# Performance work log

Measured on AMD Instinct MI355X. Metric: run time of the kernel, lower is better.

Reference implementation:

```python
import jax, jax.numpy as jnp
import numpy as np

N, E, G = 50000, 800000, 128
F_IN, F0, D, NL, DN = 128, 256, 256, 4, 512


def setup_inputs() -> dict:
    key = jax.random.key(0)
    ks = iter(jax.random.split(key, 40))

    def U(shape, fan_in):
        s = 1.0 / np.sqrt(fan_in)
        return jax.random.uniform(next(ks), shape, minval=-s, maxval=s, dtype=jnp.float32)

    x = jax.random.normal(next(ks), (N, F_IN), dtype=jnp.float32)
    edge_index = jax.random.randint(next(ks), (2, E), 0, N)
    batch_index = jnp.sort(jax.random.randint(next(ks), (N,), 0, G))
    return dict(
        x=x, edge_index=edge_index, batch_index=batch_index,
        fl_W=U((F_IN, F0), F_IN), fl_b=U((F0,), F_IN),
        conv1_W=U((F0, D), F0), conv1_b=U((D,), F0),
        tr1_W=U((D, D), D), tr1_b=U((D,), D),
        bn1_g=jnp.ones((D,), jnp.float32), bn1_b=jnp.zeros((D,), jnp.float32),
        convs_W=U((NL, D, D), D), convs_b=U((NL, D), D),
        trs_W=U((NL, D, D), D), trs_b=U((NL, D), D),
        bns_g=jnp.ones((NL, D), jnp.float32), bns_b=jnp.zeros((NL, D), jnp.float32),
        l1_W=U((2 * D, DN), 2 * D), l1_b=U((DN,), 2 * D),
        l2_W=U((DN, DN // 2), DN), l2_b=U((DN // 2,), DN),
        l3_W=U((DN // 2, 10), DN // 2), l3_b=U((10,), DN // 2),
    )


def reference(x, edge_index, batch_index, fl_W, fl_b, conv1_W, conv1_b,
              tr1_W, tr1_b, bn1_g, bn1_b, convs_W, convs_b, trs_W, trs_b,
              bns_g, bns_b, l1_W, l1_b, l2_W, l2_b, l3_W, l3_b):
    n = x.shape[0]
    loops = jnp.arange(n, dtype=edge_index.dtype)
    src = jnp.concatenate([edge_index[0], loops])  # [E+N] GCN self-loops
    dst = jnp.concatenate([edge_index[1], loops])
    deg = jax.ops.segment_sum(jnp.ones_like(dst, dtype=x.dtype), dst, num_segments=n)
    dis = jax.lax.rsqrt(deg)  # deg >= 1 due to self-loops
    norm = dis[src] * dis[dst]  # [E+N] symmetric normalization

    def gcn(h, W, b):
        m = h @ W
        return jax.ops.segment_sum(norm[:, None] * m[src], dst, num_segments=n) + b

    def bn(h, g, bb):
        mu = h.mean(axis=0)
        var = jnp.mean((h - mu) ** 2, axis=0)  # biased var, torch BN train math
        return g * (h - mu) * jax.lax.rsqrt(var + 1e-5) + bb

    h = x @ fl_W + fl_b
    h = jax.nn.relu(gcn(h, conv1_W, conv1_b))
    h = bn(h, bn1_g, bn1_b)
    h = jax.nn.relu(h @ tr1_W + tr1_b)  # dropout off (eval)
    for i in range(convs_W.shape[0]):
        h = jax.nn.relu(gcn(h, convs_W[i], convs_b[i]))
        h = bn(h, bns_g[i], bns_b[i])
        h = jax.nn.relu(h @ trs_W[i] + trs_b[i])

    sums = jax.ops.segment_sum(h, batch_index, num_segments=G)
    cnt = jax.ops.segment_sum(jnp.ones((n,), h.dtype), batch_index, num_segments=G)
    pooled = sums / jnp.maximum(cnt, 1.0)[:, None]  # global_mean_pool
    z = jnp.concatenate([pooled, pooled], axis=1)
    z = jax.nn.relu(z @ l1_W + l1_b)
    z = jax.nn.relu(z @ l2_W + l2_b)
    return z @ l3_W + l3_b
```

## Files before the change

kernel.cpp:

```cpp
#include <hip/hip_runtime.h>

#define DD 256

typedef unsigned short u16;
typedef unsigned int u32;
using bf16x8 = __attribute__((ext_vector_type(8))) short;
using f16x8  = __attribute__((ext_vector_type(8))) _Float16;
using f32x4  = __attribute__((ext_vector_type(4))) float;

#define GLB_PTR(p) ((const __attribute__((address_space(1))) u32*)(p))
#define LDS_PTR(p) ((__attribute__((address_space(3))) u32*)(p))


__device__ __forceinline__ u32 f2bfx2(float v) {
  u32 b = __float_as_uint(v);
  u32 hi = (b + 0x7fffu + ((b >> 16) & 1u)) >> 16;
  float hf = __uint_as_float(hi << 16);
  float lof = v - hf;
  u32 b2 = __float_as_uint(lof);
  u32 lo = (b2 + 0x7fffu + ((b2 >> 16) & 1u)) >> 16;
  return hi | (lo << 16);
}

__device__ __forceinline__ u16 f2h(float f) {
  _Float16 h = (_Float16)f;
  return __builtin_bit_cast(unsigned short, h);
}
__device__ __forceinline__ float h2f(u16 x) {
  return (float)__builtin_bit_cast(_Float16, x);
}

__device__ __forceinline__ bf16x8 as_bf16x8(uint4 u) {
  union { uint4 u; bf16x8 v; } c;
  c.u = u;
  return c.v;
}
__device__ __forceinline__ f16x8 as_f16x8(uint4 u) {
  union { uint4 u; f16x8 v; } c;
  c.u = u;
  return c.v;
}

__device__ __forceinline__ void unpack8(uint4 a, uint4 b, bf16x8& hi, bf16x8& lo) {
  union { u32 w[4]; bf16x8 v; } H, L;
  H.w[0] = __builtin_amdgcn_perm(a.y, a.x, 0x05040100u);
  L.w[0] = __builtin_amdgcn_perm(a.y, a.x, 0x07060302u);
  H.w[1] = __builtin_amdgcn_perm(a.w, a.z, 0x05040100u);
  L.w[1] = __builtin_amdgcn_perm(a.w, a.z, 0x07060302u);
  H.w[2] = __builtin_amdgcn_perm(b.y, b.x, 0x05040100u);
  L.w[2] = __builtin_amdgcn_perm(b.y, b.x, 0x07060302u);
  H.w[3] = __builtin_amdgcn_perm(b.w, b.z, 0x05040100u);
  L.w[3] = __builtin_amdgcn_perm(b.w, b.z, 0x07060302u);
  hi = H.v;
  lo = L.v;
}

__device__ __forceinline__ int packoff(int col, int k) {
  int w = col >> 6, r = (col >> 4) & 3, c16 = col & 15;
  int kc = k >> 5, q = (k >> 3) & 3, j = k & 7;
  return ((kc * 4 + w) * 4 + r) * 512 + (q * 16 + c16) * 8 + j;
}


__global__ void zero_i32_kernel(int* p, int n) {
  int i = blockIdx.x * 256 + threadIdx.x;
  if (i < n) p[i] = 0;
}

__global__ void zero_f32_kernel(float* p, int n) {
  int i = blockIdx.x * 256 + threadIdx.x;
  if (i < n) p[i] = 0.f;
}

__global__ void count_kernel(const int* __restrict__ dst, int* __restrict__ cnt, int e) {
  int i = blockIdx.x * 256 + threadIdx.x;
  if (i < e) atomicAdd(&cnt[dst[i]], 1);
}

__global__ void scan_block_kernel(const int* __restrict__ cnt, int* __restrict__ out,
                                  int* __restrict__ bsum, int n) {
  __shared__ int sh[256];
  int tid = threadIdx.x;
  int base = blockIdx.x * 1024 + tid * 4;
  int v0 = (base + 0 < n) ? cnt[base + 0] : 0;
  int v1 = (base + 1 < n) ? cnt[base + 1] : 0;
  int v2 = (base + 2 < n) ? cnt[base + 2] : 0;
  int v3 = (base + 3 < n) ? cnt[base + 3] : 0;
  int s = v0 + v1 + v2 + v3;
  sh[tid] = s;
  __syncthreads();
  for (int d = 1; d < 256; d <<= 1) {
    int t = (tid >= d) ? sh[tid - d] : 0;
    __syncthreads();
    sh[tid] += t;
    __syncthreads();
  }
  int excl = sh[tid] - s;
  if (base + 0 < n) out[base + 0] = excl;
  excl += v0;
  if (base + 1 < n) out[base + 1] = excl;
  excl += v1;
  if (base + 2 < n) out[base + 2] = excl;
  excl += v2;
  if (base + 3 < n) out[base + 3] = excl;
  if (tid == 255) bsum[blockIdx.x] = sh[255];
}

__global__ void scan_partials_kernel(int* bsum, int nb) {
  if (threadIdx.x == 0 && blockIdx.x == 0) {
    int acc = 0;
    for (int i = 0; i < nb; ++i) { int t = bsum[i]; bsum[i] = acc; acc += t; }
  }
}

__global__ void finalize_kernel(int* __restrict__ off, const int* __restrict__ bsum,
                                int* __restrict__ cursor, const int* __restrict__ cnt,
                                float* __restrict__ dis, int n, int e) {
  int i = blockIdx.x * 256 + threadIdx.x;
  if (i < n) {
    int o = off[i] + bsum[i >> 10];
    off[i] = o;
    cursor[i] = o;
    dis[i] = rsqrtf((float)(cnt[i] + 1));
  }
  if (i == 0 && blockIdx.x == 0) off[n] = e;
}

__global__ void fill_kernel(const int* __restrict__ src, const int* __restrict__ dst,
                            int* __restrict__ cursor, const float* __restrict__ dis,
                            int2* __restrict__ csrE, int e) {
  int i = blockIdx.x * 256 + threadIdx.x;
  if (i < e) {
    int s = src[i];
    int d = dst[i];
    int p = atomicAdd(&cursor[d], 1);
    float w = dis[s] * dis[d];
    csrE[p] = make_int2(s, __float_as_int(w));
  }
}


__global__ void xsplit_kernel(const float* __restrict__ x, u32* __restrict__ xq, int n) {
  int i = blockIdx.x * 256 + threadIdx.x;
  if (i < n) xq[i] = f2bfx2(x[i]);
}


__global__ void wsplit_all_kernel(const float* __restrict__ fl_W, const float* __restrict__ conv1_W,
                                  const float* __restrict__ convs_W, u16* __restrict__ flHi,
                                  u16* __restrict__ flLo, u16* __restrict__ cvF) {
  int j = blockIdx.x;
  int m = blockIdx.y;
  int k = threadIdx.x;
  if (m == 0) {
    if (k < 128) {
      u32 p = f2bfx2(fl_W[(size_t)k * 256 + j]);
      int off = packoff(j, k);
      flHi[off] = (u16)(p & 0xffffu);
      flLo[off] = (u16)(p >> 16);
    }
  } else {
    int c = m - 1;
    const float* W = (c == 0) ? conv1_W : convs_W + (size_t)(c - 1) * 65536;
    cvF[(size_t)c * 65536 + packoff(j, k)] = f2h(W[(size_t)k * 256 + j]);
  }
}

__global__ void wsplit_fold_kernel(const float* __restrict__ W, const float* __restrict__ scale,
                                   const float* __restrict__ shift, const float* __restrict__ bt,
                                   u16* __restrict__ trF, float* __restrict__ bias_out) {
  __shared__ float red[256];
  int j = blockIdx.x;
  int k = threadIdx.x;
  float w = W[(size_t)k * 256 + j];
  trF[packoff(j, k)] = f2h(w * scale[k]);
  red[k] = shift[k] * w;
  __syncthreads();
  for (int d = 128; d > 0; d >>= 1) {
    if (k < d) red[k] += red[k + d];
    __syncthreads();
  }
  if (k == 0) bias_out[j] = bt[j] + red[0];
}


__device__ __forceinline__ f16x8 afrag16(const u32* As, int R, int q) {
  int off = (q * 4) ^ (((R >> 1) & 3) << 2);
  return as_f16x8(*(const uint4*)(As + R * 16 + off));
}

__device__ __forceinline__ void afrag32(const u32* Asbase, int R, int q, bf16x8& ah, bf16x8& al) {
  int s = (R & 7) << 4;
  const u32* row = Asbase + R * 32;
  uint4 a0 = *(const uint4*)(row + ((((q * 32)) ^ s) >> 2));
  uint4 a1 = *(const uint4*)(row + ((((q * 32) + 16) ^ s) >> 2));
  unpack8(a0, a1, ah, al);
}

__global__ __launch_bounds__(256) void fused_fl_kernel(
    const u32* __restrict__ Aq, const u16* __restrict__ W1h, const u16* __restrict__ W1l,
    const float* __restrict__ bias1, const u16* __restrict__ W2f, u16* __restrict__ C,
    int nrows) {
  constexpr int NK1 = 4;
  __shared__ __align__(16) u32 As[2][2048];
  __shared__ __align__(16) u16 T[64 * 256];
  const int tid = threadIdx.x;
  const int lane = tid & 63;
  const int wave = tid >> 6;
  const int row0 = blockIdx.x * 64;
  const int q = lane >> 4;
  const int r16 = lane & 15;

  int sRowG[2], sOff[2];
#pragma unroll
  for (int c = 0; c < 2; ++c) {
    int row_l = c * 32 + wave * 8 + (lane >> 3);
    int grow = row0 + row_l;
    if (grow > nrows - 1) grow = nrows - 1;
    sRowG[c] = grow;
    sOff[c] = ((lane & 7) * 4) ^ ((row_l & 7) << 2);
  }

  int bBase[4];
#pragma unroll
  for (int r = 0; r < 4; ++r) bBase[r] = (wave * 4 + r) * 512 + lane * 8;

  f32x4 acc[4][4];
#pragma unroll
  for (int i = 0; i < 4; ++i)
#pragma unroll
    for (int r = 0; r < 4; ++r) acc[i][r] = (f32x4){0.f, 0.f, 0.f, 0.f};

  auto stage = [&](int buf, int kc32) {
#pragma unroll
    for (int c = 0; c < 2; ++c) {
      const u32* gsrc = Aq + (size_t)sRowG[c] * 128 + kc32 * 32 + sOff[c];
      u32* ldst = &As[buf][c * 1024 + wave * 256];
      __builtin_amdgcn_global_load_lds(GLB_PTR(gsrc), LDS_PTR(ldst), 16, 0, 0);
    }
  };

  stage(0, 0);
  __syncthreads();
  int buf = 0;
#pragma unroll
  for (int kc = 0; kc < NK1; ++kc) {
    if (kc + 1 < NK1) stage(buf ^ 1, kc + 1);
    uint4 BH[4], BL[4];
#pragma unroll
    for (int r = 0; r < 4; ++r) {
      BH[r] = *(const uint4*)(W1h + bBase[r] + kc * 8192);
      BL[r] = *(const uint4*)(W1l + bBase[r] + kc * 8192);
    }
    bf16x8 ah[4], al[4];
#pragma unroll
    for (int i = 0; i < 4; ++i) afrag32(As[buf], i * 16 + r16, q, ah[i], al[i]);
#pragma unroll
    for (int r = 0; r < 4; ++r) {
      bf16x8 bh = as_bf16x8(BH[r]);
      bf16x8 bl = as_bf16x8(BL[r]);
#pragma unroll
      for (int i = 0; i < 4; ++i) {
        acc[i][r] = __builtin_amdgcn_mfma_f32_16x16x32_bf16(ah[i], bh, acc[i][r], 0, 0, 0);
        acc[i][r] = __builtin_amdgcn_mfma_f32_16x16x32_bf16(al[i], bh, acc[i][r], 0, 0, 0);
        acc[i][r] = __builtin_amdgcn_mfma_f32_16x16x32_bf16(ah[i], bl, acc[i][r], 0, 0, 0);
      }
    }
    __syncthreads();
    buf ^= 1;
  }

#pragma unroll
  for (int r = 0; r < 4; ++r) {
    int col = wave * 64 + r * 16 + r16;
    float bv = bias1[col];
#pragma unroll
    for (int i = 0; i < 4; ++i) {
#pragma unroll
      for (int g = 0; g < 4; ++g) {
        int row = i * 16 + q * 4 + g;
        float v = acc[i][r][g] + bv;
        *(u16*)((char*)T + row * 512 + ((col * 2) ^ ((row & 7) << 4))) = f2h(v);
      }
    }
  }

#pragma unroll
  for (int i = 0; i < 4; ++i)
#pragma unroll
    for (int r = 0; r < 4; ++r) acc[i][r] = (f32x4){0.f, 0.f, 0.f, 0.f};
  __syncthreads();

#pragma unroll
  for (int kc = 0; kc < 8; ++kc) {
    uint4 BF[4];
#pragma unroll
    for (int r = 0; r < 4; ++r) BF[r] = *(const uint4*)(W2f + bBase[r] + kc * 8192);
    f16x8 af[4];
#pragma unroll
    for (int i = 0; i < 4; ++i) {
      int row = i * 16 + r16;
      int base = kc * 64 + q * 16;
      af[i] = as_f16x8(*(const uint4*)((char*)T + row * 512 + (base ^ ((row & 7) << 4))));
    }
#pragma unroll
    for (int r = 0; r < 4; ++r) {
      f16x8 bf = as_f16x8(BF[r]);
#pragma unroll
      for (int i = 0; i < 4; ++i)
        acc[i][r] = __builtin_amdgcn_mfma_f32_16x16x32_f16(af[i], bf, acc[i][r], 0, 0, 0);
    }
  }

#pragma unroll
  for (int r = 0; r < 4; ++r) {
    int col = wave * 64 + r * 16 + r16;
#pragma unroll
    for (int i = 0; i < 4; ++i) {
#pragma unroll
      for (int g = 0; g < 4; ++g) {
        int row = row0 + i * 16 + q * 4 + g;
        if (row < nrows) C[(size_t)row * 256 + col] = f2h(acc[i][r][g]);
      }
    }
  }
}

__global__ __launch_bounds__(256) void fused_h_kernel(
    const u16* __restrict__ Ah, const u16* __restrict__ W1f, const float* __restrict__ bias1,
    const u16* __restrict__ W2f, u16* __restrict__ C, int nrows) {
  __shared__ __align__(16) u32 As[2][1024];
  __shared__ __align__(16) u16 T[64 * 256];
  const int tid = threadIdx.x;
  const int lane = tid & 63;
  const int wave = tid >> 6;
  const int row0 = blockIdx.x * 64;
  const int q = lane >> 4;
  const int r16 = lane & 15;

  int row_l = tid >> 2;
  int grow = row0 + row_l;
  if (grow > nrows - 1) grow = nrows - 1;
  const int sK = (((tid & 3) * 8)) ^ (((row_l >> 1) & 3) << 3);

  int bBase[4];
#pragma unroll
  for (int r = 0; r < 4; ++r) bBase[r] = (wave * 4 + r) * 512 + lane * 8;

  f32x4 acc[4][4];
#pragma unroll
  for (int i = 0; i < 4; ++i)
#pragma unroll
    for (int r = 0; r < 4; ++r) acc[i][r] = (f32x4){0.f, 0.f, 0.f, 0.f};

  auto stage = [&](int buf, int kc32) {
    const u16* gsrc = Ah + (size_t)grow * 256 + kc32 * 32 + sK;
    u32* ldst = &As[buf][wave * 256];
    __builtin_amdgcn_global_load_lds(GLB_PTR(gsrc), LDS_PTR(ldst), 16, 0, 0);
  };

  stage(0, 0);
  __syncthreads();
  int buf = 0;
#pragma unroll
  for (int kc = 0; kc < 8; ++kc) {
    if (kc + 1 < 8) stage(buf ^ 1, kc + 1);
    uint4 BF[4];
#pragma unroll
    for (int r = 0; r < 4; ++r) BF[r] = *(const uint4*)(W1f + bBase[r] + kc * 8192);
    f16x8 af[4];
#pragma unroll
    for (int i = 0; i < 4; ++i) af[i] = afrag16(As[buf], i * 16 + r16, q);
#pragma unroll
    for (int r = 0; r < 4; ++r) {
      f16x8 bf = as_f16x8(BF[r]);
#pragma unroll
      for (int i = 0; i < 4; ++i)
        acc[i][r] = __builtin_amdgcn_mfma_f32_16x16x32_f16(af[i], bf, acc[i][r], 0, 0, 0);
    }
    __syncthreads();
    buf ^= 1;
  }

#pragma unroll
  for (int r = 0; r < 4; ++r) {
    int col = wave * 64 + r * 16 + r16;
    float bv = bias1[col];
#pragma unroll
    for (int i = 0; i < 4; ++i) {
#pragma unroll
      for (int g = 0; g < 4; ++g) {
        int row = i * 16 + q * 4 + g;
        float v = fmaxf(acc[i][r][g] + bv, 0.f);
        *(u16*)((char*)T + row * 512 + ((col * 2) ^ ((row & 7) << 4))) = f2h(v);
      }
    }
  }

#pragma unroll
  for (int i = 0; i < 4; ++i)
#pragma unroll
    for (int r = 0; r < 4; ++r) acc[i][r] = (f32x4){0.f, 0.f, 0.f, 0.f};
  __syncthreads();

#pragma unroll
  for (int kc = 0; kc < 8; ++kc) {
    uint4 BF[4];
#pragma unroll
    for (int r = 0; r < 4; ++r) BF[r] = *(const uint4*)(W2f + bBase[r] + kc * 8192);
    f16x8 af[4];
#pragma unroll
    for (int i = 0; i < 4; ++i) {
      int row = i * 16 + r16;
      int base = kc * 64 + q * 16;
      af[i] = as_f16x8(*(const uint4*)((char*)T + row * 512 + (base ^ ((row & 7) << 4))));
    }
#pragma unroll
    for (int r = 0; r < 4; ++r) {
      f16x8 bf = as_f16x8(BF[r]);
#pragma unroll
      for (int i = 0; i < 4; ++i)
        acc[i][r] = __builtin_amdgcn_mfma_f32_16x16x32_f16(af[i], bf, acc[i][r], 0, 0, 0);
    }
  }

#pragma unroll
  for (int r = 0; r < 4; ++r) {
    int col = wave * 64 + r * 16 + r16;
#pragma unroll
    for (int i = 0; i < 4; ++i) {
#pragma unroll
      for (int g = 0; g < 4; ++g) {
        int row = row0 + i * 16 + q * 4 + g;
        if (row < nrows) C[(size_t)row * 256 + col] = f2h(acc[i][r][g]);
      }
    }
  }
}

__global__ __launch_bounds__(256) void gemm_h_kernel(
    const u16* __restrict__ Ah, const u16* __restrict__ W1f, const float* __restrict__ bias,
    u16* __restrict__ C, int nrows) {
  __shared__ __align__(16) u32 As[2][1024];
  const int tid = threadIdx.x;
  const int lane = tid & 63;
  const int wave = tid >> 6;
  const int row0 = blockIdx.x * 64;
  const int q = lane >> 4;
  const int r16 = lane & 15;

  int row_l = tid >> 2;
  int grow = row0 + row_l;
  if (grow > nrows - 1) grow = nrows - 1;
  const int sK = (((tid & 3) * 8)) ^ (((row_l >> 1) & 3) << 3);

  int bBase[4];
#pragma unroll
  for (int r = 0; r < 4; ++r) bBase[r] = (wave * 4 + r) * 512 + lane * 8;

  f32x4 acc[4][4];
#pragma unroll
  for (int i = 0; i < 4; ++i)
#pragma unroll
    for (int r = 0; r < 4; ++r) acc[i][r] = (f32x4){0.f, 0.f, 0.f, 0.f};

  auto stage = [&](int buf, int kc32) {
    const u16* gsrc = Ah + (size_t)grow * 256 + kc32 * 32 + sK;
    u32* ldst = &As[buf][wave * 256];
    __builtin_amdgcn_global_load_lds(GLB_PTR(gsrc), LDS_PTR(ldst), 16, 0, 0);
  };

  stage(0, 0);
  __syncthreads();
  int buf = 0;
#pragma unroll
  for (int kc = 0; kc < 8; ++kc) {
    if (kc + 1 < 8) stage(buf ^ 1, kc + 1);
    uint4 BF[4];
#pragma unroll
    for (int r = 0; r < 4; ++r) BF[r] = *(const uint4*)(W1f + bBase[r] + kc * 8192);
    f16x8 af[4];
#pragma unroll
    for (int i = 0; i < 4; ++i) af[i] = afrag16(As[buf], i * 16 + r16, q);
#pragma unroll
    for (int r = 0; r < 4; ++r) {
      f16x8 bf = as_f16x8(BF[r]);
#pragma unroll
      for (int i = 0; i < 4; ++i)
        acc[i][r] = __builtin_amdgcn_mfma_f32_16x16x32_f16(af[i], bf, acc[i][r], 0, 0, 0);
    }
    __syncthreads();
    buf ^= 1;
  }

#pragma unroll
  for (int r = 0; r < 4; ++r) {
    int col = wave * 64 + r * 16 + r16;
    float bv = bias[col];
#pragma unroll
    for (int i = 0; i < 4; ++i) {
#pragma unroll
      for (int g = 0; g < 4; ++g) {
        int row = row0 + i * 16 + q * 4 + g;
        if (row < nrows) C[(size_t)row * 256 + col] = f2h(fmaxf(acc[i][r][g] + bv, 0.f));
      }
    }
  }
}


__global__ __launch_bounds__(256) void gather_kernel(
    const u16* __restrict__ m, const int* __restrict__ off,
    const int2* __restrict__ csrE, const float* __restrict__ dis,
    const float* __restrict__ bias, u16* __restrict__ out,
    float* __restrict__ shard, int n) {
  __shared__ float2 red[4][256];
  int wv = threadIdx.x >> 6;
  int lane = threadIdx.x & 63;
  int node = blockIdx.x * 4 + wv;
  float ax = 0.f, ay = 0.f, az = 0.f, aw = 0.f;
  if (node < n) {
    float di = dis[node];
    uint2 v = *(const uint2*)(m + (size_t)node * DD + lane * 4);
    float w = di * di;
    ax = w * h2f((u16)(v.x & 0xffff)); ay = w * h2f((u16)(v.x >> 16));
    az = w * h2f((u16)(v.y & 0xffff)); aw = w * h2f((u16)(v.y >> 16));
    int e0 = off[node], e1 = off[node + 1];
    int e = e0;
    for (; e + 3 < e1; e += 4) {
      int2 p0 = csrE[e], p1 = csrE[e + 1], p2 = csrE[e + 2], p3 = csrE[e + 3];
      float w0 = __int_as_float(p0.y), w1 = __int_as_float(p1.y);
      float w2 = __int_as_float(p2.y), w3 = __int_as_float(p3.y);
      uint2 u0 = *(const uint2*)(m + (size_t)p0.x * DD + lane * 4);
      uint2 u1 = *(const uint2*)(m + (size_t)p1.x * DD + lane * 4);
      uint2 u2 = *(const uint2*)(m + (size_t)p2.x * DD + lane * 4);
      uint2 u3 = *(const uint2*)(m + (size_t)p3.x * DD + lane * 4);
      ax = fmaf(w0, h2f((u16)(u0.x & 0xffff)), ax); ay = fmaf(w0, h2f((u16)(u0.x >> 16)), ay);
      az = fmaf(w0, h2f((u16)(u0.y & 0xffff)), az); aw = fmaf(w0, h2f((u16)(u0.y >> 16)), aw);
      ax = fmaf(w1, h2f((u16)(u1.x & 0xffff)), ax); ay = fmaf(w1, h2f((u16)(u1.x >> 16)), ay);
      az = fmaf(w1, h2f((u16)(u1.y & 0xffff)), az); aw = fmaf(w1, h2f((u16)(u1.y >> 16)), aw);
      ax = fmaf(w2, h2f((u16)(u2.x & 0xffff)), ax); ay = fmaf(w2, h2f((u16)(u2.x >> 16)), ay);
      az = fmaf(w2, h2f((u16)(u2.y & 0xffff)), az); aw = fmaf(w2, h2f((u16)(u2.y >> 16)), aw);
      ax = fmaf(w3, h2f((u16)(u3.x & 0xffff)), ax); ay = fmaf(w3, h2f((u16)(u3.x >> 16)), ay);
      az = fmaf(w3, h2f((u16)(u3.y & 0xffff)), az); aw = fmaf(w3, h2f((u16)(u3.y >> 16)), aw);
    }
    for (; e < e1; ++e) {
      int2 p0 = csrE[e];
      float w0 = __int_as_float(p0.y);
      uint2 u0 = *(const uint2*)(m + (size_t)p0.x * DD + lane * 4);
      ax = fmaf(w0, h2f((u16)(u0.x & 0xffff)), ax); ay = fmaf(w0, h2f((u16)(u0.x >> 16)), ay);
      az = fmaf(w0, h2f((u16)(u0.y & 0xffff)), az); aw = fmaf(w0, h2f((u16)(u0.y >> 16)), aw);
    }
    float4 bb = *(const float4*)(bias + lane * 4);
    ax = fmaxf(ax + bb.x, 0.f);
    ay = fmaxf(ay + bb.y, 0.f);
    az = fmaxf(az + bb.z, 0.f);
    aw = fmaxf(aw + bb.w, 0.f);
    uint2 oo;
    oo.x = (u32)f2h(ax) | ((u32)f2h(ay) << 16);
    oo.y = (u32)f2h(az) | ((u32)f2h(aw) << 16);
    *(uint2*)(out + (size_t)node * DD + lane * 4) = oo;
  }
  red[wv][lane * 4 + 0] = make_float2(ax, ax * ax);
  red[wv][lane * 4 + 1] = make_float2(ay, ay * ay);
  red[wv][lane * 4 + 2] = make_float2(az, az * az);
  red[wv][lane * 4 + 3] = make_float2(aw, aw * aw);
  __syncthreads();
  int c = threadIdx.x;
  float2 a = red[0][c], b2 = red[1][c], c2 = red[2][c], d2 = red[3][c];
  float s = (a.x + b2.x) + (c2.x + d2.x);
  float qq = (a.y + b2.y) + (c2.y + d2.y);
  float* sh = shard + (size_t)(blockIdx.x & 63) * 512;
  atomicAdd(&sh[c], s);
  atomicAdd(&sh[256 + c], qq);
}


__global__ void bn_finalize_kernel(const float* __restrict__ shard, const float* __restrict__ g,
                                   const float* __restrict__ b, float* __restrict__ scale,
                                   float* __restrict__ shift, float inv_n) {
  int c = threadIdx.x;
  float s = 0.f, q = 0.f;
  for (int i = 0; i < 64; ++i) {
    s += shard[(size_t)i * 512 + c];
    q += shard[(size_t)i * 512 + 256 + c];
  }
  float mu = s * inv_n;
  float var = q * inv_n - mu * mu;
  float inv = rsqrtf(var + 1e-5f);
  float sc = g[c] * inv;
  scale[c] = sc;
  shift[c] = b[c] - mu * sc;
}


__global__ void pool_kernel(const u16* __restrict__ h, const int* __restrict__ batch,
                            float* __restrict__ pooled, int n) {
  int g = blockIdx.x;
  int c = threadIdx.x;
  int lo = 0, hi = n;
  while (lo < hi) { int mid = (lo + hi) >> 1; if (batch[mid] < g) lo = mid + 1; else hi = mid; }
  int start = lo;
  hi = n;
  while (lo < hi) { int mid = (lo + hi) >> 1; if (batch[mid] <= g) lo = mid + 1; else hi = mid; }
  int end = lo;
  float a0 = 0.f, a1 = 0.f, a2 = 0.f, a3 = 0.f;
  int r = start;
  for (; r + 3 < end; r += 4) {
    a0 += h2f(h[(size_t)(r + 0) * DD + c]);
    a1 += h2f(h[(size_t)(r + 1) * DD + c]);
    a2 += h2f(h[(size_t)(r + 2) * DD + c]);
    a3 += h2f(h[(size_t)(r + 3) * DD + c]);
  }
  for (; r < end; ++r) a0 += h2f(h[(size_t)r * DD + c]);
  float s = (a0 + a1) + (a2 + a3);
  int cg = end - start;
  pooled[g * DD + c] = s / (float)(cg > 1 ? cg : 1);
}


__global__ void mlp1_kernel(const float* __restrict__ pooled, const float* __restrict__ W,
                            const float* __restrict__ b, float* __restrict__ out) {
  __shared__ float p[256];
  int g = blockIdx.x;
  int j = blockIdx.y * 256 + threadIdx.x;
  p[threadIdx.x] = pooled[g * 256 + threadIdx.x];
  __syncthreads();
  float acc = b[j];
#pragma unroll 8
  for (int k = 0; k < 512; ++k) acc = fmaf(p[k & 255], W[k * 512 + j], acc);
  out[g * 512 + j] = fmaxf(acc, 0.f);
}

__global__ void mlp2_kernel(const float* __restrict__ z1, const float* __restrict__ W,
                            const float* __restrict__ b, float* __restrict__ out) {
  __shared__ float p[512];
  int g = blockIdx.x;
  p[threadIdx.x] = z1[g * 512 + threadIdx.x];
  p[256 + threadIdx.x] = z1[g * 512 + 256 + threadIdx.x];
  __syncthreads();
  float acc = b[threadIdx.x];
#pragma unroll 8
  for (int k = 0; k < 512; ++k) acc = fmaf(p[k], W[k * 256 + threadIdx.x], acc);
  out[g * 256 + threadIdx.x] = fmaxf(acc, 0.f);
}

__global__ void mlp3_kernel(const float* __restrict__ z2, const float* __restrict__ W,
                            const float* __restrict__ b, float* __restrict__ out) {
  int g = blockIdx.x;
  int lane = threadIdx.x;
  float acc[10];
#pragma unroll
  for (int o = 0; o < 10; ++o) acc[o] = 0.f;
  for (int k = lane; k < 256; k += 64) {
    float v = z2[g * 256 + k];
#pragma unroll
    for (int o = 0; o < 10; ++o) acc[o] = fmaf(v, W[k * 10 + o], acc[o]);
  }
#pragma unroll
  for (int o = 0; o < 10; ++o) {
    float s = acc[o];
    for (int d = 32; d > 0; d >>= 1) s += __shfl_down(s, d);
    if (lane == 0) out[g * 10 + o] = s + b[o];
  }
}


extern "C" void kernel_launch(void* const* d_in, const int* in_sizes, int n_in,
                              void* d_out, int out_size, void* d_ws, size_t ws_size,
                              hipStream_t stream) {
  const float* x = (const float*)d_in[0];
  const int* ei = (const int*)d_in[1];
  const int* batch = (const int*)d_in[2];
  const float* fl_W = (const float*)d_in[3];
  const float* fl_b = (const float*)d_in[4];
  const float* conv1_W = (const float*)d_in[5];
  const float* conv1_b = (const float*)d_in[6];
  const float* tr1_W = (const float*)d_in[7];
  const float* tr1_b = (const float*)d_in[8];
  const float* bn1_g = (const float*)d_in[9];
  const float* bn1_b = (const float*)d_in[10];
  const float* convs_W = (const float*)d_in[11];
  const float* convs_b = (const float*)d_in[12];
  const float* trs_W = (const float*)d_in[13];
  const float* trs_b = (const float*)d_in[14];
  const float* bns_g = (const float*)d_in[15];
  const float* bns_b = (const float*)d_in[16];
  const float* l1_W = (const float*)d_in[17];
  const float* l1_b = (const float*)d_in[18];
  const float* l2_W = (const float*)d_in[19];
  const float* l2_b = (const float*)d_in[20];
  const float* l3_W = (const float*)d_in[21];
  const float* l3_b = (const float*)d_in[22];

  const int N = in_sizes[0] / 128;
  const int E = in_sizes[1] / 2;
  const int G = out_size / 10;
  const int NL = in_sizes[11] / (256 * 256);
  const int* src = ei;
  const int* dst = ei + E;

  char* ws = (char*)d_ws;
  size_t o = 0;
  auto alloc = [&](size_t bytes) -> char* {
    o = (o + 255) & ~(size_t)255;
    char* p = ws + o;
    o += bytes;
    return p;
  };
  u16* hA = (u16*)alloc((size_t)N * DD * 2);
  u16* mF = (u16*)alloc((size_t)N * DD * 2);
  u32* xq = (u32*)alloc((size_t)N * 128 * 4);
  float* dis = (float*)alloc((size_t)N * 4);
  int* cnt = (int*)alloc((size_t)N * 4);
  int* off = (int*)alloc((size_t)(N + 1) * 4);
  int* cursor = (int*)alloc((size_t)N * 4);
  int* bsum = (int*)alloc(64 * 4);
  int2* csrE = (int2*)alloc((size_t)E * 8);
  float* shards = (float*)alloc((size_t)(1 + NL) * 64 * 512 * 4);
  float* scalev = (float*)alloc(256 * 4);
  float* shiftv = (float*)alloc(256 * 4);
  float* pooled = (float*)alloc((size_t)G * 256 * 4);
  float* z1 = (float*)alloc((size_t)G * 512 * 4);
  float* z2 = (float*)alloc((size_t)G * 256 * 4);
  u16* flHi = (u16*)alloc(128 * 256 * 2);
  u16* flLo = (u16*)alloc(128 * 256 * 2);
  u16* cvF = (u16*)alloc((size_t)(1 + NL) * 256 * 256 * 2);
  u16* trF = (u16*)alloc(256 * 256 * 2);
  float* trBias = (float*)alloc(256 * 4);

  dim3 b256(256);
  const int nblk = (N + 63) / 64;

  zero_i32_kernel<<<(N + 255) / 256, b256, 0, stream>>>(cnt, N);
  count_kernel<<<(E + 255) / 256, b256, 0, stream>>>(dst, cnt, E);
  int nb = (N + 1023) / 1024;
  scan_block_kernel<<<nb, b256, 0, stream>>>(cnt, off, bsum, N);
  scan_partials_kernel<<<1, 64, 0, stream>>>(bsum, nb);
  finalize_kernel<<<(N + 255) / 256, b256, 0, stream>>>(off, bsum, cursor, cnt, dis, N, E);
  fill_kernel<<<(E + 255) / 256, b256, 0, stream>>>(src, dst, cursor, dis, csrE, E);

  xsplit_kernel<<<(N * 128 + 255) / 256, b256, 0, stream>>>(x, xq, N * 128);
  dim3 wgrid(256, 2 + NL);
  wsplit_all_kernel<<<wgrid, b256, 0, stream>>>(fl_W, conv1_W, convs_W, flHi, flLo, cvF);
  int shard_elems = (1 + NL) * 64 * 512;
  zero_f32_kernel<<<(shard_elems + 255) / 256, b256, 0, stream>>>(shards, shard_elems);

  fused_fl_kernel<<<nblk, b256, 0, stream>>>(xq, flHi, flLo, fl_b, cvF, mF, N);

  for (int L = 0; L < 1 + NL; ++L) {
    const float* bc = (L == 0) ? conv1_b : convs_b + (size_t)(L - 1) * 256;
    const float* gg = (L == 0) ? bn1_g : bns_g + (size_t)(L - 1) * 256;
    const float* gb = (L == 0) ? bn1_b : bns_b + (size_t)(L - 1) * 256;
    const float* Wt = (L == 0) ? tr1_W : trs_W + (size_t)(L - 1) * 256 * 256;
    const float* bt = (L == 0) ? tr1_b : trs_b + (size_t)(L - 1) * 256;
    float* slot = shards + (size_t)L * 64 * 512;

    gather_kernel<<<(N + 3) / 4, b256, 0, stream>>>(mF, off, csrE, dis, bc, hA, slot, N);
    bn_finalize_kernel<<<1, b256, 0, stream>>>(slot, gg, gb, scalev, shiftv, 1.0f / (float)N);
    wsplit_fold_kernel<<<256, b256, 0, stream>>>(Wt, scalev, shiftv, bt, trF, trBias);
    if (L < NL) {
      fused_h_kernel<<<nblk, b256, 0, stream>>>(hA, trF, trBias,
                                                cvF + (size_t)(L + 1) * 65536, mF, N);
    } else {
      gemm_h_kernel<<<nblk, b256, 0, stream>>>(hA, trF, trBias, mF, N);
    }
  }

  pool_kernel<<<G, b256, 0, stream>>>(mF, batch, pooled, N);
  dim3 m1grid(G, 2);
  mlp1_kernel<<<m1grid, b256, 0, stream>>>(pooled, l1_W, l1_b, z1);
  mlp2_kernel<<<G, b256, 0, stream>>>(z1, l2_W, l2_b, z2);
  mlp3_kernel<<<G, 64, 0, stream>>>(z2, l3_W, l3_b, (float*)d_out);
}
```

Before: 750.5 us.

## Fuse BN finalize into weight fold, widen GEMM K staging, unroll gather by 8

```diff
diff --git a/kernel.cpp b/kernel.cpp
--- a/kernel.cpp
+++ b/kernel.cpp
@@ -166,15 +166,27 @@
   }
 }
 
-__global__ void wsplit_fold_kernel(const float* __restrict__ W, const float* __restrict__ scale,
-                                   const float* __restrict__ shift, const float* __restrict__ bt,
-                                   u16* __restrict__ trF, float* __restrict__ bias_out) {
+__global__ void wsplit_fold_kernel(const float* __restrict__ W, const float* __restrict__ shard,
+                                   const float* __restrict__ g, const float* __restrict__ b,
+                                   const float* __restrict__ bt, u16* __restrict__ trF,
+                                   float* __restrict__ bias_out, float inv_n) {
   __shared__ float red[256];
   int j = blockIdx.x;
   int k = threadIdx.x;
+  float s = 0.f, q = 0.f;
+#pragma unroll 8
+  for (int i = 0; i < 64; ++i) {
+    s += shard[(size_t)i * 512 + k];
+    q += shard[(size_t)i * 512 + 256 + k];
+  }
+  float mu = s * inv_n;
+  float var = q * inv_n - mu * mu;
+  float inv = rsqrtf(var + 1e-5f);
+  float sc = g[k] * inv;
+  float sh = b[k] - mu * sc;
   float w = W[(size_t)k * 256 + j];
-  trF[packoff(j, k)] = f2h(w * scale[k]);
-  red[k] = shift[k] * w;
+  trF[packoff(j, k)] = f2h(w * sc);
+  red[k] = sh * w;
   __syncthreads();
   for (int d = 128; d > 0; d >>= 1) {
     if (k < d) red[k] += red[k + d];
@@ -183,11 +195,6 @@
   if (k == 0) bias_out[j] = bt[j] + red[0];
 }
 
-
-__device__ __forceinline__ f16x8 afrag16(const u32* As, int R, int q) {
-  int off = (q * 4) ^ (((R >> 1) & 3) << 2);
-  return as_f16x8(*(const uint4*)(As + R * 16 + off));
-}
 
 __device__ __forceinline__ void afrag32(const u32* Asbase, int R, int q, bf16x8& ah, bf16x8& al) {
   int s = (R & 7) << 4;
@@ -195,6 +202,11 @@
   uint4 a0 = *(const uint4*)(row + ((((q * 32)) ^ s) >> 2));
   uint4 a1 = *(const uint4*)(row + ((((q * 32) + 16) ^ s) >> 2));
   unpack8(a0, a1, ah, al);
+}
+
+__device__ __forceinline__ f16x8 afrag64(const u32* As, int R, int ch, int q) {
+  int s = (ch * 4 + q) ^ (R & 7);
+  return as_f16x8(*(const uint4*)(As + R * 32 + s * 4));
 }
 
 __global__ __launch_bounds__(256) void fused_fl_kernel(
@@ -329,7 +341,7 @@
 __global__ __launch_bounds__(256) void fused_h_kernel(
     const u16* __restrict__ Ah, const u16* __restrict__ W1f, const float* __restrict__ bias1,
     const u16* __restrict__ W2f, u16* __restrict__ C, int nrows) {
-  __shared__ __align__(16) u32 As[2][1024];
+  __shared__ __align__(16) u32 As[2][2048];
   __shared__ __align__(16) u16 T[64 * 256];
   const int tid = threadIdx.x;
   const int lane = tid & 63;
@@ -338,10 +350,15 @@
   const int q = lane >> 4;
   const int r16 = lane & 15;
 
-  int row_l = tid >> 2;
-  int grow = row0 + row_l;
-  if (grow > nrows - 1) grow = nrows - 1;
-  const int sK = (((tid & 3) * 8)) ^ (((row_l >> 1) & 3) << 3);
+  int sRowG[2], sOffH[2];
+#pragma unroll
+  for (int c = 0; c < 2; ++c) {
+    int row_l = c * 32 + wave * 8 + (lane >> 3);
+    int grow = row0 + row_l;
+    if (grow > nrows - 1) grow = nrows - 1;
+    sRowG[c] = grow;
+    sOffH[c] = ((lane & 7) ^ (row_l & 7)) * 8;
+  }
 
   int bBase[4];
 #pragma unroll
@@ -353,30 +370,37 @@
 #pragma unroll
     for (int r = 0; r < 4; ++r) acc[i][r] = (f32x4){0.f, 0.f, 0.f, 0.f};
 
-  auto stage = [&](int buf, int kc32) {
-    const u16* gsrc = Ah + (size_t)grow * 256 + kc32 * 32 + sK;
-    u32* ldst = &As[buf][wave * 256];
-    __builtin_amdgcn_global_load_lds(GLB_PTR(gsrc), LDS_PTR(ldst), 16, 0, 0);
+  auto stage = [&](int buf, int kc64) {
+#pragma unroll
+    for (int c = 0; c < 2; ++c) {
+      const u16* gsrc = Ah + (size_t)sRowG[c] * 256 + kc64 * 64 + sOffH[c];
+      u32* ldst = &As[buf][c * 1024 + wave * 256];
+      __builtin_amdgcn_global_load_lds(GLB_PTR(gsrc), LDS_PTR(ldst), 16, 0, 0);
+    }
   };
 
   stage(0, 0);
   __syncthreads();
   int buf = 0;
 #pragma unroll
-  for (int kc = 0; kc < 8; ++kc) {
-    if (kc + 1 < 8) stage(buf ^ 1, kc + 1);
-    uint4 BF[4];
-#pragma unroll
-    for (int r = 0; r < 4; ++r) BF[r] = *(const uint4*)(W1f + bBase[r] + kc * 8192);
-    f16x8 af[4];
-#pragma unroll
-    for (int i = 0; i < 4; ++i) af[i] = afrag16(As[buf], i * 16 + r16, q);
-#pragma unroll
-    for (int r = 0; r < 4; ++r) {
-      f16x8 bf = as_f16x8(BF[r]);
-#pragma unroll
-      for (int i = 0; i < 4; ++i)
-        acc[i][r] = __builtin_amdgcn_mfma_f32_16x16x32_f16(af[i], bf, acc[i][r], 0, 0, 0);
+  for (int kc = 0; kc < 4; ++kc) {
+    if (kc + 1 < 4) stage(buf ^ 1, kc + 1);
+#pragma unroll
+    for (int ch = 0; ch < 2; ++ch) {
+      int kc32 = kc * 2 + ch;
+      uint4 BF[4];
+#pragma unroll
+      for (int r = 0; r < 4; ++r) BF[r] = *(const uint4*)(W1f + bBase[r] + kc32 * 8192);
+      f16x8 af[4];
+#pragma unroll
+      for (int i = 0; i < 4; ++i) af[i] = afrag64(As[buf], i * 16 + r16, ch, q);
+#pragma unroll
+      for (int r = 0; r < 4; ++r) {
+        f16x8 bf = as_f16x8(BF[r]);
+#pragma unroll
+        for (int i = 0; i < 4; ++i)
+          acc[i][r] = __builtin_amdgcn_mfma_f32_16x16x32_f16(af[i], bf, acc[i][r], 0, 0, 0);
+      }
     }
     __syncthreads();
     buf ^= 1;
@@ -441,7 +465,7 @@
 __global__ __launch_bounds__(256) void gemm_h_kernel(
     const u16* __restrict__ Ah, const u16* __restrict__ W1f, const float* __restrict__ bias,
     u16* __restrict__ C, int nrows) {
-  __shared__ __align__(16) u32 As[2][1024];
+  __shared__ __align__(16) u32 As[2][2048];
   const int tid = threadIdx.x;
   const int lane = tid & 63;
   const int wave = tid >> 6;
@@ -449,10 +473,15 @@
   const int q = lane >> 4;
   const int r16 = lane & 15;
 
-  int row_l = tid >> 2;
-  int grow = row0 + row_l;
-  if (grow > nrows - 1) grow = nrows - 1;
-  const int sK = (((tid & 3) * 8)) ^ (((row_l >> 1) & 3) << 3);
+  int sRowG[2], sOffH[2];
+#pragma unroll
+  for (int c = 0; c < 2; ++c) {
+    int row_l = c * 32 + wave * 8 + (lane >> 3);
+    int grow = row0 + row_l;
+    if (grow > nrows - 1) grow = nrows - 1;
+    sRowG[c] = grow;
+    sOffH[c] = ((lane & 7) ^ (row_l & 7)) * 8;
+  }
 
   int bBase[4];
 #pragma unroll
@@ -464,30 +493,37 @@
 #pragma unroll
     for (int r = 0; r < 4; ++r) acc[i][r] = (f32x4){0.f, 0.f, 0.f, 0.f};
 
-  auto stage = [&](int buf, int kc32) {
-    const u16* gsrc = Ah + (size_t)grow * 256 + kc32 * 32 + sK;
-    u32* ldst = &As[buf][wave * 256];
-    __builtin_amdgcn_global_load_lds(GLB_PTR(gsrc), LDS_PTR(ldst), 16, 0, 0);
+  auto stage = [&](int buf, int kc64) {
+#pragma unroll
+    for (int c = 0; c < 2; ++c) {
+      const u16* gsrc = Ah + (size_t)sRowG[c] * 256 + kc64 * 64 + sOffH[c];
+      u32* ldst = &As[buf][c * 1024 + wave * 256];
+      __builtin_amdgcn_global_load_lds(GLB_PTR(gsrc), LDS_PTR(ldst), 16, 0, 0);
+    }
   };
 
   stage(0, 0);
   __syncthreads();
   int buf = 0;
 #pragma unroll
-  for (int kc = 0; kc < 8; ++kc) {
-    if (kc + 1 < 8) stage(buf ^ 1, kc + 1);
-    uint4 BF[4];
-#pragma unroll
-    for (int r = 0; r < 4; ++r) BF[r] = *(const uint4*)(W1f + bBase[r] + kc * 8192);
-    f16x8 af[4];
-#pragma unroll
-    for (int i = 0; i < 4; ++i) af[i] = afrag16(As[buf], i * 16 + r16, q);
-#pragma unroll
-    for (int r = 0; r < 4; ++r) {
-      f16x8 bf = as_f16x8(BF[r]);
-#pragma unroll
-      for (int i = 0; i < 4; ++i)
-        acc[i][r] = __builtin_amdgcn_mfma_f32_16x16x32_f16(af[i], bf, acc[i][r], 0, 0, 0);
+  for (int kc = 0; kc < 4; ++kc) {
+    if (kc + 1 < 4) stage(buf ^ 1, kc + 1);
+#pragma unroll
+    for (int ch = 0; ch < 2; ++ch) {
+      int kc32 = kc * 2 + ch;
+      uint4 BF[4];
+#pragma unroll
+      for (int r = 0; r < 4; ++r) BF[r] = *(const uint4*)(W1f + bBase[r] + kc32 * 8192);
+      f16x8 af[4];
+#pragma unroll
+      for (int i = 0; i < 4; ++i) af[i] = afrag64(As[buf], i * 16 + r16, ch, q);
+#pragma unroll
+      for (int r = 0; r < 4; ++r) {
+        f16x8 bf = as_f16x8(BF[r]);
+#pragma unroll
+        for (int i = 0; i < 4; ++i)
+          acc[i][r] = __builtin_amdgcn_mfma_f32_16x16x32_f16(af[i], bf, acc[i][r], 0, 0, 0);
+      }
     }
     __syncthreads();
     buf ^= 1;
@@ -525,24 +561,38 @@
     float w = di * di;
     ax = w * h2f((u16)(v.x & 0xffff)); ay = w * h2f((u16)(v.x >> 16));
     az = w * h2f((u16)(v.y & 0xffff)); aw = w * h2f((u16)(v.y >> 16));
-    int e0 = off[node], e1 = off[node + 1];
-    int e = e0;
+    int e = off[node], e1 = off[node + 1];
+    for (; e + 7 < e1; e += 8) {
+      int2 p[8];
+#pragma unroll
+      for (int j = 0; j < 8; ++j) p[j] = csrE[e + j];
+      uint2 u[8];
+#pragma unroll
+      for (int j = 0; j < 8; ++j) u[j] = *(const uint2*)(m + (size_t)p[j].x * DD + lane * 4);
+#pragma unroll
+      for (int j = 0; j < 8; ++j) {
+        float ww = __int_as_float(p[j].y);
+        ax = fmaf(ww, h2f((u16)(u[j].x & 0xffff)), ax);
+        ay = fmaf(ww, h2f((u16)(u[j].x >> 16)), ay);
+        az = fmaf(ww, h2f((u16)(u[j].y & 0xffff)), az);
+        aw = fmaf(ww, h2f((u16)(u[j].y >> 16)), aw);
+      }
+    }
     for (; e + 3 < e1; e += 4) {
-      int2 p0 = csrE[e], p1 = csrE[e + 1], p2 = csrE[e + 2], p3 = csrE[e + 3];
-      float w0 = __int_as_float(p0.y), w1 = __int_as_float(p1.y);
-      float w2 = __int_as_float(p2.y), w3 = __int_as_float(p3.y);
-      uint2 u0 = *(const uint2*)(m + (size_t)p0.x * DD + lane * 4);
-      uint2 u1 = *(const uint2*)(m + (size_t)p1.x * DD + lane * 4);
-      uint2 u2 = *(const uint2*)(m + (size_t)p2.x * DD + lane * 4);
-      uint2 u3 = *(const uint2*)(m + (size_t)p3.x * DD + lane * 4);
-      ax = fmaf(w0, h2f((u16)(u0.x & 0xffff)), ax); ay = fmaf(w0, h2f((u16)(u0.x >> 16)), ay);
-      az = fmaf(w0, h2f((u16)(u0.y & 0xffff)), az); aw = fmaf(w0, h2f((u16)(u0.y >> 16)), aw);
-      ax = fmaf(w1, h2f((u16)(u1.x & 0xffff)), ax); ay = fmaf(w1, h2f((u16)(u1.x >> 16)), ay);
-      az = fmaf(w1, h2f((u16)(u1.y & 0xffff)), az); aw = fmaf(w1, h2f((u16)(u1.y >> 16)), aw);
-      ax = fmaf(w2, h2f((u16)(u2.x & 0xffff)), ax); ay = fmaf(w2, h2f((u16)(u2.x >> 16)), ay);
-      az = fmaf(w2, h2f((u16)(u2.y & 0xffff)), az); aw = fmaf(w2, h2f((u16)(u2.y >> 16)), aw);
-      ax = fmaf(w3, h2f((u16)(u3.x & 0xffff)), ax); ay = fmaf(w3, h2f((u16)(u3.x >> 16)), ay);
-      az = fmaf(w3, h2f((u16)(u3.y & 0xffff)), az); aw = fmaf(w3, h2f((u16)(u3.y >> 16)), aw);
+      int2 p[4];
+#pragma unroll
+      for (int j = 0; j < 4; ++j) p[j] = csrE[e + j];
+      uint2 u[4];
+#pragma unroll
+      for (int j = 0; j < 4; ++j) u[j] = *(const uint2*)(m + (size_t)p[j].x * DD + lane * 4);
+#pragma unroll
+      for (int j = 0; j < 4; ++j) {
+        float ww = __int_as_float(p[j].y);
+        ax = fmaf(ww, h2f((u16)(u[j].x & 0xffff)), ax);
+        ay = fmaf(ww, h2f((u16)(u[j].x >> 16)), ay);
+        az = fmaf(ww, h2f((u16)(u[j].y & 0xffff)), az);
+        aw = fmaf(ww, h2f((u16)(u[j].y >> 16)), aw);
+      }
     }
     for (; e < e1; ++e) {
       int2 p0 = csrE[e];
@@ -573,24 +623,6 @@
   float* sh = shard + (size_t)(blockIdx.x & 63) * 512;
   atomicAdd(&sh[c], s);
   atomicAdd(&sh[256 + c], qq);
-}
-
-
-__global__ void bn_finalize_kernel(const float* __restrict__ shard, const float* __restrict__ g,
-                                   const float* __restrict__ b, float* __restrict__ scale,
-                                   float* __restrict__ shift, float inv_n) {
-  int c = threadIdx.x;
-  float s = 0.f, q = 0.f;
-  for (int i = 0; i < 64; ++i) {
-    s += shard[(size_t)i * 512 + c];
-    q += shard[(size_t)i * 512 + 256 + c];
-  }
-  float mu = s * inv_n;
-  float var = q * inv_n - mu * mu;
-  float inv = rsqrtf(var + 1e-5f);
-  float sc = g[c] * inv;
-  scale[c] = sc;
-  shift[c] = b[c] - mu * sc;
 }
 
 
@@ -718,8 +750,6 @@
   int* bsum = (int*)alloc(64 * 4);
   int2* csrE = (int2*)alloc((size_t)E * 8);
   float* shards = (float*)alloc((size_t)(1 + NL) * 64 * 512 * 4);
-  float* scalev = (float*)alloc(256 * 4);
-  float* shiftv = (float*)alloc(256 * 4);
   float* pooled = (float*)alloc((size_t)G * 256 * 4);
   float* z1 = (float*)alloc((size_t)G * 512 * 4);
   float* z2 = (float*)alloc((size_t)G * 256 * 4);
@@ -757,8 +787,8 @@
     float* slot = shards + (size_t)L * 64 * 512;
 
     gather_kernel<<<(N + 3) / 4, b256, 0, stream>>>(mF, off, csrE, dis, bc, hA, slot, N);
-    bn_finalize_kernel<<<1, b256, 0, stream>>>(slot, gg, gb, scalev, shiftv, 1.0f / (float)N);
-    wsplit_fold_kernel<<<256, b256, 0, stream>>>(Wt, scalev, shiftv, bt, trF, trBias);
+    wsplit_fold_kernel<<<256, b256, 0, stream>>>(Wt, slot, gg, gb, bt, trF, trBias,
+                                                 1.0f / (float)N);
     if (L < NL) {
       fused_h_kernel<<<nblk, b256, 0, stream>>>(hA, trF, trBias,
                                                 cvF + (size_t)(L + 1) * 65536, mF, N);
```

Measured after the change: 738.3 us. Within noise of the previous version (-1.6%).
